# Kernel tuning notes

Measured on AMD Instinct MI355X. Metric: run time of the kernel, lower is better.

Reference implementation:

```python
import jax, jax.numpy as jnp
import numpy as np

B, T, C = 4, 2048, 1024
N_HEAD = 16
HEAD_DIM = C // N_HEAD


def setup_inputs() -> dict:
    key = jax.random.key(0)
    k1, k2, k3 = jax.random.split(key, 3)
    x = jax.random.normal(k1, (B, T, C), dtype=jnp.float32)
    w_attn = jax.random.normal(k2, (C, 3 * C), dtype=jnp.float32) * 0.02
    b_attn = jnp.zeros((3 * C,), dtype=jnp.float32)
    # c_proj init stddev = 0.02 / sqrt(2 * n_layer), n_layer = 24
    w_proj = jax.random.normal(k3, (C, C), dtype=jnp.float32) * (0.02 / np.sqrt(48.0))
    b_proj = jnp.zeros((C,), dtype=jnp.float32)
    return {"x": x, "w_attn": w_attn, "b_attn": b_attn,
            "w_proj": w_proj, "b_proj": b_proj}


def reference(x, w_attn, b_attn, w_proj, b_proj):
    Bx, Tx, Cx = x.shape
    scale = 1.0 / jnp.sqrt(jnp.asarray(HEAD_DIM, dtype=x.dtype))
    qkv = x @ w_attn + b_attn                      # [B,T,3C]
    qkv = qkv.reshape(Bx, Tx, 3, N_HEAD, HEAD_DIM)
    q, k, v = qkv[:, :, 0], qkv[:, :, 1], qkv[:, :, 2]  # each [B,T,H,D]
    att = jnp.einsum('bthd,bThd->bhtT', q, k) * scale   # [B,H,T,T]
    mask = jnp.tril(jnp.ones((Tx, Tx), dtype=x.dtype)).reshape(1, 1, Tx, Tx)
    att = att * mask - 1e10 * (1 - mask)
    att = jax.nn.softmax(att, axis=-1)
    y = jnp.einsum('bhtT,bThd->bthd', att, v)      # [B,T,H,D]
    y = y.reshape(Bx, Tx, Cx)
    return y @ w_proj + b_proj
```

## Files before the change

### kernel.cpp

```cpp
#include <hip/hip_runtime.h>
#include <hip/hip_bf16.h>


typedef __attribute__((ext_vector_type(8)))  __bf16 bf16x8;
typedef __attribute__((ext_vector_type(4)))  float  f32x4;
typedef __attribute__((ext_vector_type(16))) float  f32x16;
typedef __attribute__((ext_vector_type(4)))  unsigned int u32x4;

#define AS1C(p) ((const __attribute__((address_space(1))) unsigned int*)(p))
#define AS3(p)  ((__attribute__((address_space(3))) unsigned int*)(p))

__device__ __forceinline__ unsigned short f2bfu(float f){
  __hip_bfloat16 h = __float2bfloat16(f);
  return __builtin_bit_cast(unsigned short, h);
}

__device__ __forceinline__ void plswapu(unsigned int &a, unsigned int &b){
  asm("v_permlane32_swap_b32 %0, %1" : "+v"(a), "+v"(b));
}
__device__ __forceinline__ unsigned int cvtpk(float lo, float hi){
  unsigned int r;
  asm("v_cvt_pk_bf16_f32 %0, %1, %2" : "=v"(r) : "v"(lo), "v"(hi));
  return r;
}
__device__ __forceinline__ float max3f(float a, float b, float c){
  float r;
  asm("v_max3_f32 %0, %1, %2, %3" : "=v"(r) : "v"(a), "v"(b), "v"(c));
  return r;
}


__global__ __launch_bounds__(256)
void f32_to_bf16_vec(const float* __restrict__ in, __hip_bfloat16* __restrict__ out, int n4){
  int stride = gridDim.x * blockDim.x;
  for (int i = blockIdx.x*blockDim.x + threadIdx.x; i < n4; i += stride){
    float4 v = reinterpret_cast<const float4*>(in)[i];
    ushort4 u;
    u.x = f2bfu(v.x); u.y = f2bfu(v.y); u.z = f2bfu(v.z); u.w = f2bfu(v.w);
    reinterpret_cast<ushort4*>(out)[i] = u;
  }
}

__global__ __launch_bounds__(256)
void transpose_to_bf16(const float* __restrict__ in, __hip_bfloat16* __restrict__ out, int R, int C){
  __shared__ float tile[32][33];
  const int tx = threadIdx.x & 31, ty = threadIdx.x >> 5;
  const int c0 = blockIdx.x*32, r0 = blockIdx.y*32;
  for (int i = ty; i < 32; i += 8)
    tile[i][tx] = in[(size_t)(r0+i)*C + c0 + tx];
  __syncthreads();
  for (int i = ty; i < 32; i += 8)
    out[(size_t)(c0+i)*R + r0 + tx] = __float2bfloat16(tile[tx][i]);
}


#define QSCALE 0.1803368801111244f

__device__ __forceinline__ void stage_ab(const __hip_bfloat16* __restrict__ A,
                                         const __hip_bfloat16* __restrict__ Bt,
                                         int m0, int n0, int K, int kt,
                                         __hip_bfloat16* sA, __hip_bfloat16* sB,
                                         int w, int l)
{
  const int k0 = kt*32;
  #pragma unroll
  for (int qq = 0; qq < 2; ++qq){
    const int c = qq*256 + w*64 + l;
    const int row = c>>2, kc = c&3;
    __builtin_amdgcn_global_load_lds(AS1C(A  + (size_t)(m0+row)*K + k0 + 8*kc),
                                     AS3(sA + (qq*256 + w*64)*8), 16, 0, 0);
    __builtin_amdgcn_global_load_lds(AS1C(Bt + (size_t)(n0+row)*K + k0 + 8*kc),
                                     AS3(sB + (qq*256 + w*64)*8), 16, 0, 0);
  }
}

template<int EPI>
__global__ __launch_bounds__(256)
void gemm_bf16(const __hip_bfloat16* __restrict__ A,
               const __hip_bfloat16* __restrict__ Bt,
               const float* __restrict__ bias,
               int M, int N, int K,
               __hip_bfloat16* __restrict__ q_s,
               __hip_bfloat16* __restrict__ k_s,
               __hip_bfloat16* __restrict__ vT_s,
               float* __restrict__ outf)
{
  __shared__ __align__(16) __hip_bfloat16 sA[2][128*32];
  __shared__ __align__(16) __hip_bfloat16 sB[2][128*32];
  const int tid = threadIdx.x, w = tid>>6, l = tid&63, g = l>>4, li = l&15;
  const int wm = w>>1, wn = w&1;

  const int nwg = gridDim.x, cpx = nwg >> 3;
  const int swz = (blockIdx.x & 7)*cpx + (blockIdx.x >> 3);
  const int nbx = N >> 7;
  const int m0 = (swz / nbx)*128, n0 = (swz % nbx)*128;

  f32x4 acc[4][4] = {};

  const int NT = K >> 5;
  stage_ab(A, Bt, m0, n0, K, 0, sA[0], sB[0], w, l);
  int cur = 0;

  for (int kt = 0; kt < NT; ++kt){
    __syncthreads();
    if (kt + 1 < NT)
      stage_ab(A, Bt, m0, n0, K, kt+1, sA[cur^1], sB[cur^1], w, l);

    bf16x8 af[4], bfr[4];
    #pragma unroll
    for (int mi = 0; mi < 4; ++mi)
      af[mi] = *reinterpret_cast<const bf16x8*>(sA[cur] + (wm*64 + mi*16 + li)*32 + 8*g);
    #pragma unroll
    for (int ni = 0; ni < 4; ++ni)
      bfr[ni] = *reinterpret_cast<const bf16x8*>(sB[cur] + (wn*64 + ni*16 + li)*32 + 8*g);
    #pragma unroll
    for (int mi = 0; mi < 4; ++mi)
      #pragma unroll
      for (int ni = 0; ni < 4; ++ni)
        acc[mi][ni] = __builtin_amdgcn_mfma_f32_16x16x32_bf16(af[mi], bfr[ni], acc[mi][ni], 0, 0, 0);
    cur ^= 1;
  }

  #pragma unroll
  for (int ni = 0; ni < 4; ++ni){
    const int col = n0 + wn*64 + ni*16 + li;
    const float bv = bias[col];
    #pragma unroll
    for (int mi = 0; mi < 4; ++mi){
      #pragma unroll
      for (int e = 0; e < 4; ++e){
        const int row = m0 + wm*64 + mi*16 + 4*g + e;
        const float val = acc[mi][ni][e] + bv;
        if (EPI == 0){
          const int three = col >> 10, h = (col >> 6) & 15, d = col & 63;
          const int b = row >> 11, t = row & 2047;
          const int bh = b*16 + h;
          if (three == 0)      q_s[((size_t)bh*2048 + t)*64 + d]  = __float2bfloat16(val*QSCALE);
          else if (three == 1) k_s[((size_t)bh*2048 + t)*64 + d]  = __float2bfloat16(val);
          else                 vT_s[((size_t)bh*64 + d)*2048 + t] = __float2bfloat16(val);
        } else {
          outf[(size_t)row*N + col] = val;
        }
      }
    }
  }
}


__device__ __forceinline__ void stage_kv64(const __hip_bfloat16* __restrict__ k_s,
                                           const __hip_bfloat16* __restrict__ vT_s,
                                           size_t base, int j,
                                           __hip_bfloat16* sk, __hip_bfloat16* svt,
                                           int tid)
{
  #pragma unroll
  for (int it = 0; it < 4; ++it){
    const int c = it*128 + tid;
    const int r = c>>3, cc = c&7;
    __builtin_amdgcn_global_load_lds(AS1C(k_s  + base + (size_t)(j*64 + r)*64 + 8*(cc ^ (r&7))),
                                     AS3(sk  + c*8), 16, 0, 0);
    __builtin_amdgcn_global_load_lds(AS1C(vT_s + base + (size_t)r*2048 + j*64 + 8*(cc ^ (r&7))),
                                     AS3(svt + c*8), 16, 0, 0);
  }
}

__device__ __forceinline__ bf16x8 ldtile(const __hip_bfloat16* t, int row, int chunk){
  return *reinterpret_cast<const bf16x8*>(t + row*64 + ((chunk ^ (row&7))*8));
}

__global__ __launch_bounds__(128, 3)
void flash_attn(const __hip_bfloat16* __restrict__ q_s,
                const __hip_bfloat16* __restrict__ k_s,
                const __hip_bfloat16* __restrict__ vT_s,
                __hip_bfloat16* __restrict__ y_s)
{
  __shared__ __align__(16) __hip_bfloat16 sk [2][64*64];
  __shared__ __align__(16) __hip_bfloat16 svt[2][64*64];

  const int tid = threadIdx.x, w = tid>>6, l = tid&63;
  const int lq = l&31, hf = l>>5, h4 = 4*hf;
  const int bid = blockIdx.x;
  const int xcd = bid & 7, sl = (bid>>3) & 7;
  const int v = 31 - (bid >> 6);
  const int bh = xcd*8 + sl;
  const size_t base = (size_t)bh * (2048*64);
  const int b = bh >> 4, hh = bh & 15;

  const int tw = 2*v + w;
  const int jd = v;
  const int qabs = 32*tw + lq;
  const int rel = 32*w + lq;

  bf16x8 qf[4];
  #pragma unroll
  for (int ks = 0; ks < 4; ++ks)
    qf[ks] = *reinterpret_cast<const bf16x8*>(q_s + base + (size_t)qabs*64 + 16*ks + 8*hf);

  f32x16 o0 = {}, o1 = {};
  float mrun = -1e30f, lrun = 0.f;

  stage_kv64(k_s, vT_s, base, 0, sk[0], svt[0], tid);

  #pragma unroll 1
  for (int j = 0; j <= jd; ++j){
    __syncthreads();
    if (j + 1 <= jd)
      stage_kv64(k_s, vT_s, base, j+1, sk[(j+1)&1], svt[(j+1)&1], tid);

    const __hip_bfloat16* skc  = sk[j&1];
    const __hip_bfloat16* svtc = svt[j&1];

    f32x16 s0 = {}, s1 = {};
    __builtin_amdgcn_s_setprio(1);
    #pragma unroll
    for (int ks = 0; ks < 4; ++ks){
      bf16x8 kf0 = ldtile(skc, lq,      2*ks + hf);
      s0 = __builtin_amdgcn_mfma_f32_32x32x16_bf16(kf0, qf[ks], s0, 0, 0, 0);
      bf16x8 kf1 = ldtile(skc, 32 + lq, 2*ks + hf);
      s1 = __builtin_amdgcn_mfma_f32_32x32x16_bf16(kf1, qf[ks], s1, 0, 0, 0);
    }
    __builtin_amdgcn_s_setprio(0);

    if (j == jd){
      #pragma unroll
      for (int r = 0; r < 16; ++r){
        const int kv0 = (r&3) + 8*(r>>2) + h4;
        s0[r] = (kv0      <= rel) ? s0[r] : -1e30f;
        s1[r] = (kv0 + 32 <= rel) ? s1[r] : -1e30f;
      }
    }

    #define PFX(K) (((K) < 16) ? s0[K] : s1[(K)-16])
    float t0 = max3f(PFX(0),PFX(1),PFX(2)),   t1 = max3f(PFX(3),PFX(4),PFX(5));
    float t2 = max3f(PFX(6),PFX(7),PFX(8)),   t3 = max3f(PFX(9),PFX(10),PFX(11));
    float t4 = max3f(PFX(12),PFX(13),PFX(14)),t5 = max3f(PFX(15),PFX(16),PFX(17));
    float t6 = max3f(PFX(18),PFX(19),PFX(20)),t7 = max3f(PFX(21),PFX(22),PFX(23));
    float t8 = max3f(PFX(24),PFX(25),PFX(26)),t9 = max3f(PFX(27),PFX(28),PFX(29));
    float t10 = fmaxf(PFX(30),PFX(31));
    float u0 = max3f(t0,t1,t2), u1 = max3f(t3,t4,t5), u2 = max3f(t6,t7,t8);
    float u3 = fmaxf(t9,t10);
    float pm = fmaxf(max3f(u0,u1,u2), u3);
    #undef PFX

    if (!__all(pm - mrun <= 8.0f)){
      pm = fmaxf(pm, __shfl_xor(pm, 32));
      const float nm = fmaxf(mrun, pm);
      const float corr = exp2f(mrun - nm);
      mrun = nm;
      o0 *= corr; o1 *= corr;
      lrun *= corr;
    }

    #pragma unroll
    for (int r = 0; r < 16; ++r){
      s0[r] = exp2f(s0[r] - mrun);
      s1[r] = exp2f(s1[r] - mrun);
    }

    float c16[16];
    #pragma unroll
    for (int k = 0; k < 16; ++k) c16[k] = s0[k] + s1[k];
    float d8[8];
    #pragma unroll
    for (int k = 0; k < 8; ++k) d8[k] = c16[k] + c16[k+8];
    float d4a = d8[0]+d8[4], d4b = d8[1]+d8[5], d4c = d8[2]+d8[6], d4d = d8[3]+d8[7];
    float psum = (d4a+d4c) + (d4b+d4d);
    psum += __shfl_xor(psum, 32);
    lrun += psum;

    unsigned int wds[16];
    #pragma unroll
    for (int k = 0; k < 8; ++k) wds[k]   = cvtpk(s0[2*k], s0[2*k+1]);
    #pragma unroll
    for (int k = 0; k < 8; ++k) wds[8+k] = cvtpk(s1[2*k], s1[2*k+1]);
    #pragma unroll
    for (int a = 0; a < 2; ++a)
      #pragma unroll
      for (int bl = 0; bl < 2; ++bl){
        plswapu(wds[a*8 + 4*bl    ], wds[a*8 + 4*bl + 2]);
        plswapu(wds[a*8 + 4*bl + 1], wds[a*8 + 4*bl + 3]);
      }
    bf16x8 pfr[4];
    #pragma unroll
    for (int B = 0; B < 4; ++B){
      u32x4 tt = { wds[4*B], wds[4*B+1], wds[4*B+2], wds[4*B+3] };
      pfr[B] = __builtin_bit_cast(bf16x8, tt);
    }

    __builtin_amdgcn_s_setprio(1);
    #pragma unroll
    for (int ks = 0; ks < 4; ++ks){
      bf16x8 vf0 = ldtile(svtc, lq,      2*ks + hf);
      o0 = __builtin_amdgcn_mfma_f32_32x32x16_bf16(vf0, pfr[ks], o0, 0, 0, 0);
      bf16x8 vf1 = ldtile(svtc, 32 + lq, 2*ks + hf);
      o1 = __builtin_amdgcn_mfma_f32_32x32x16_bf16(vf1, pfr[ks], o1, 0, 0, 0);
    }
    __builtin_amdgcn_s_setprio(0);
  }

  const float inv = 1.f / lrun;
  __hip_bfloat16* yp = y_s + ((size_t)(b*2048 + qabs))*1024 + hh*64;
  #pragma unroll
  for (int i = 0; i < 8; ++i){
    const int d = (2*i & 3) + 8*(i>>1) + h4;
    *reinterpret_cast<unsigned int*>(yp + d)      = cvtpk(o0[2*i]*inv, o0[2*i+1]*inv);
    *reinterpret_cast<unsigned int*>(yp + 32 + d) = cvtpk(o1[2*i]*inv, o1[2*i+1]*inv);
  }
}


extern "C" void kernel_launch(void* const* d_in, const int* in_sizes, int n_in,
                              void* d_out, int out_size, void* d_ws, size_t ws_size,
                              hipStream_t stream)
{
  const float* x      = (const float*)d_in[0];
  const float* w_attn = (const float*)d_in[1];
  const float* b_attn = (const float*)d_in[2];
  const float* w_proj = (const float*)d_in[3];
  const float* b_proj = (const float*)d_in[4];
  float* out = (float*)d_out;
  char* ws = (char*)d_ws;

  __hip_bfloat16* xb     = (__hip_bfloat16*)(ws + 0);
  __hip_bfloat16* wattnT = (__hip_bfloat16*)(ws + 16777216);
  __hip_bfloat16* wprojT = (__hip_bfloat16*)(ws + 23068672);
  __hip_bfloat16* q_s    = (__hip_bfloat16*)(ws + 25165824);
  __hip_bfloat16* k_s    = (__hip_bfloat16*)(ws + 41943040);
  __hip_bfloat16* vT_s   = (__hip_bfloat16*)(ws + 58720256);
  __hip_bfloat16* y_s    = xb;

  f32_to_bf16_vec<<<2048, 256, 0, stream>>>(x, xb, 8388608/4);
  transpose_to_bf16<<<dim3(3072/32, 1024/32), 256, 0, stream>>>(w_attn, wattnT, 1024, 3072);
  transpose_to_bf16<<<dim3(1024/32, 1024/32), 256, 0, stream>>>(w_proj, wprojT, 1024, 1024);

  gemm_bf16<0><<<1536, 256, 0, stream>>>(
      xb, wattnT, b_attn, 8192, 3072, 1024, q_s, k_s, vT_s, (float*)nullptr);

  flash_attn<<<2048, 128, 0, stream>>>(q_s, k_s, vT_s, y_s);

  gemm_bf16<1><<<512, 256, 0, stream>>>(
      y_s, wprojT, b_proj, 8192, 1024, 1024,
      (__hip_bfloat16*)nullptr, (__hip_bfloat16*)nullptr, (__hip_bfloat16*)nullptr, out);
}
```

Before: 212.4 us.

## Swizzle GEMM LDS layout, group tile order, pack softmax math into float2

The GEMM staging now XOR-swizzles the 16-byte k-chunk per row, both in the global-to-LDS load and in the fragment reads, to cut LDS bank conflicts. Tile-to-block mapping is regrouped so that four consecutive blocks along M share an N column, aiming for better L2 reuse. The attention softmax is restructured around float2 vectors so the compiler can emit packed FP32 subtract and add instructions for the max-subtraction and the row sums. The swizzle has to match exactly between the store path and the read path, and the packed form may change register pressure.

```diff
diff --git a/kernel.cpp b/kernel.cpp
--- a/kernel.cpp
+++ b/kernel.cpp
@@ -3,6 +3,7 @@
 
 
 typedef __attribute__((ext_vector_type(8)))  __bf16 bf16x8;
+typedef __attribute__((ext_vector_type(2)))  float  f32x2;
 typedef __attribute__((ext_vector_type(4)))  float  f32x4;
 typedef __attribute__((ext_vector_type(16))) float  f32x16;
 typedef __attribute__((ext_vector_type(4)))  unsigned int u32x4;
@@ -67,9 +68,10 @@
   for (int qq = 0; qq < 2; ++qq){
     const int c = qq*256 + w*64 + l;
     const int row = c>>2, kc = c&3;
-    __builtin_amdgcn_global_load_lds(AS1C(A  + (size_t)(m0+row)*K + k0 + 8*kc),
+    const int kcs = kc ^ ((row>>1)&3);
+    __builtin_amdgcn_global_load_lds(AS1C(A  + (size_t)(m0+row)*K + k0 + 8*kcs),
                                      AS3(sA + (qq*256 + w*64)*8), 16, 0, 0);
-    __builtin_amdgcn_global_load_lds(AS1C(Bt + (size_t)(n0+row)*K + k0 + 8*kc),
+    __builtin_amdgcn_global_load_lds(AS1C(Bt + (size_t)(n0+row)*K + k0 + 8*kcs),
                                      AS3(sB + (qq*256 + w*64)*8), 16, 0, 0);
   }
 }
@@ -89,11 +91,15 @@
   __shared__ __align__(16) __hip_bfloat16 sB[2][128*32];
   const int tid = threadIdx.x, w = tid>>6, l = tid&63, g = l>>4, li = l&15;
   const int wm = w>>1, wn = w&1;
+  const int sw = (li>>1)&3;
 
   const int nwg = gridDim.x, cpx = nwg >> 3;
   const int swz = (blockIdx.x & 7)*cpx + (blockIdx.x >> 3);
   const int nbx = N >> 7;
-  const int m0 = (swz / nbx)*128, n0 = (swz % nbx)*128;
+  const int GM = 4, chunk = GM * nbx;
+  const int grp = swz / chunk, pos = swz - grp*chunk;
+  const int m0 = (grp*GM + (pos & (GM-1)))*128;
+  const int n0 = (pos >> 2)*128;
 
   f32x4 acc[4][4] = {};
 
@@ -109,10 +115,10 @@
     bf16x8 af[4], bfr[4];
     #pragma unroll
     for (int mi = 0; mi < 4; ++mi)
-      af[mi] = *reinterpret_cast<const bf16x8*>(sA[cur] + (wm*64 + mi*16 + li)*32 + 8*g);
+      af[mi] = *reinterpret_cast<const bf16x8*>(sA[cur] + (wm*64 + mi*16 + li)*32 + 8*(g ^ sw));
     #pragma unroll
     for (int ni = 0; ni < 4; ++ni)
-      bfr[ni] = *reinterpret_cast<const bf16x8*>(sB[cur] + (wn*64 + ni*16 + li)*32 + 8*g);
+      bfr[ni] = *reinterpret_cast<const bf16x8*>(sB[cur] + (wn*64 + ni*16 + li)*32 + 8*(g ^ sw));
     #pragma unroll
     for (int mi = 0; mi < 4; ++mi)
       #pragma unroll
@@ -221,16 +227,25 @@
     }
     __builtin_amdgcn_s_setprio(0);
 
+    f32x2 pf2[16];
+    #pragma unroll
+    for (int i = 0; i < 8; ++i){
+      pf2[i]     = (f32x2){ s0[2*i], s0[2*i+1] };
+      pf2[8 + i] = (f32x2){ s1[2*i], s1[2*i+1] };
+    }
     if (j == jd){
       #pragma unroll
-      for (int r = 0; r < 16; ++r){
-        const int kv0 = (r&3) + 8*(r>>2) + h4;
-        s0[r] = (kv0      <= rel) ? s0[r] : -1e30f;
-        s1[r] = (kv0 + 32 <= rel) ? s1[r] : -1e30f;
+      for (int i = 0; i < 16; ++i){
+        const int a = i >> 3;
+        const int r0 = (i & 7)*2, r1 = r0 + 1;
+        const int kv0 = 32*a + (r0&3) + 8*(r0>>2) + h4;
+        const int kv1 = 32*a + (r1&3) + 8*(r1>>2) + h4;
+        pf2[i].x = (kv0 <= rel) ? pf2[i].x : -1e30f;
+        pf2[i].y = (kv1 <= rel) ? pf2[i].y : -1e30f;
       }
     }
 
-    #define PFX(K) (((K) < 16) ? s0[K] : s1[(K)-16])
+    #define PFX(K) (((K)&1) ? pf2[(K)>>1].y : pf2[(K)>>1].x)
     float t0 = max3f(PFX(0),PFX(1),PFX(2)),   t1 = max3f(PFX(3),PFX(4),PFX(5));
     float t2 = max3f(PFX(6),PFX(7),PFX(8)),   t3 = max3f(PFX(9),PFX(10),PFX(11));
     float t4 = max3f(PFX(12),PFX(13),PFX(14)),t5 = max3f(PFX(15),PFX(16),PFX(17));
@@ -251,28 +266,28 @@
       lrun *= corr;
     }
 
-    #pragma unroll
-    for (int r = 0; r < 16; ++r){
-      s0[r] = exp2f(s0[r] - mrun);
-      s1[r] = exp2f(s1[r] - mrun);
-    }
-
-    float c16[16];
-    #pragma unroll
-    for (int k = 0; k < 16; ++k) c16[k] = s0[k] + s1[k];
-    float d8[8];
-    #pragma unroll
-    for (int k = 0; k < 8; ++k) d8[k] = c16[k] + c16[k+8];
-    float d4a = d8[0]+d8[4], d4b = d8[1]+d8[5], d4c = d8[2]+d8[6], d4d = d8[3]+d8[7];
-    float psum = (d4a+d4c) + (d4b+d4d);
+    const f32x2 negm = { -mrun, -mrun };
+    #pragma unroll
+    for (int i = 0; i < 16; ++i) pf2[i] = pf2[i] + negm;
+    #pragma unroll
+    for (int i = 0; i < 16; ++i){
+      pf2[i].x = exp2f(pf2[i].x);
+      pf2[i].y = exp2f(pf2[i].y);
+    }
+
+    f32x2 q8[8];
+    #pragma unroll
+    for (int i = 0; i < 8; ++i) q8[i] = pf2[i] + pf2[8+i];
+    f32x2 q4a = q8[0]+q8[4], q4b = q8[1]+q8[5], q4c = q8[2]+q8[6], q4d = q8[3]+q8[7];
+    f32x2 q2a = q4a+q4c, q2b = q4b+q4d;
+    f32x2 q1 = q2a+q2b;
+    float psum = q1.x + q1.y;
     psum += __shfl_xor(psum, 32);
     lrun += psum;
 
     unsigned int wds[16];
     #pragma unroll
-    for (int k = 0; k < 8; ++k) wds[k]   = cvtpk(s0[2*k], s0[2*k+1]);
-    #pragma unroll
-    for (int k = 0; k < 8; ++k) wds[8+k] = cvtpk(s1[2*k], s1[2*k+1]);
+    for (int k = 0; k < 16; ++k) wds[k] = cvtpk(pf2[k].x, pf2[k].y);
     #pragma unroll
     for (int a = 0; a < 2; ++a)
       #pragma unroll
```

New measurement: 204.1 us. 3.9% less time.
